# Kernel optimization log

Hardware: AMD Instinct MI355X
Metric: run time of the kernel (lower is better)

Reference implementation:

```python
import jax, jax.numpy as jnp
import numpy as np

B, T, C = 128, 64, 66
S, L, W = 512, 2, 32  # state_size, num_layers, window_size


def _gru_cell(x, h, Wih, Whh, bih, bhh):
    # PyTorch GRU cell. x:[B,in], h:[B,S]; gate order r,z,n.
    gi = x @ Wih.T + bih  # [B,3S]
    gh = h @ Whh.T + bhh
    ir, iz, inn = jnp.split(gi, 3, axis=-1)
    hr, hz, hn = jnp.split(gh, 3, axis=-1)
    r = jax.nn.sigmoid(ir + hr)
    z = jax.nn.sigmoid(iz + hz)
    n = jnp.tanh(inn + r * hn)
    return (1.0 - z) * n + z * h


def setup_inputs() -> dict:
    key = jax.random.key(0)
    ks = jax.random.split(key, 14)
    sc = 0.02
    inp = {
        'x': jax.random.normal(ks[0], (B, T, C), dtype=jnp.float32),
        'Wih0': jax.random.normal(ks[1], (3 * S, C), dtype=jnp.float32) * sc,
        'Whh0': jax.random.normal(ks[2], (3 * S, S), dtype=jnp.float32) * sc,
        'bih0': jax.random.normal(ks[3], (3 * S,), dtype=jnp.float32) * sc,
        'bhh0': jax.random.normal(ks[4], (3 * S,), dtype=jnp.float32) * sc,
        'Wih1': jax.random.normal(ks[5], (3 * S, S), dtype=jnp.float32) * sc,
        'Whh1': jax.random.normal(ks[6], (3 * S, S), dtype=jnp.float32) * sc,
        'bih1': jax.random.normal(ks[7], (3 * S,), dtype=jnp.float32) * sc,
        'bhh1': jax.random.normal(ks[8], (3 * S,), dtype=jnp.float32) * sc,
        'Wt': jax.random.normal(ks[9], (1, W), dtype=jnp.float32) * sc,   # temporal_fc_last: Linear(W,1)
        'bt': jnp.zeros((1,), dtype=jnp.float32),
        'Ws': jax.random.normal(ks[10], (C, S), dtype=jnp.float32) * sc,  # spatial_fc: Linear(S,C)
        'bs': jnp.zeros((C,), dtype=jnp.float32),
    }
    return inp


def reference(x, Wih0, Whh0, bih0, bhh0, Wih1, Whh1, bih1, bhh1, Wt, bt, Ws, bs):
    Bx, Tx, Cx = x.shape
    h0 = jnp.zeros((Bx, S), dtype=x.dtype)
    h1 = jnp.zeros((Bx, S), dtype=x.dtype)

    def stack_step(h0, h1, xt):
        h0 = _gru_cell(xt, h0, Wih0, Whh0, bih0, bhh0)
        h1 = _gru_cell(h0, h1, Wih1, Whh1, bih1, bhh1)
        return h0, h1

    # ---- encoder over x[:, :-1, :] ----
    def enc_step(carry, xt):
        h0, h1 = stack_step(carry[0], carry[1], xt)
        return (h0, h1), h1

    (h0, h1), enc_out = jax.lax.scan(enc_step, (h0, h1), x[:, :-1, :].transpose(1, 0, 2))
    # enc_out: [T-1, B, S]; sliding window of the last W encoder outputs: [B, W, S]
    window = enc_out[-W:].transpose(1, 0, 2)

    def dec_step(carry, _):
        h0, h1, win, dinp = carry  # dinp: [B, C]
        h0, h1 = stack_step(h0, h1, dinp)
        win = jnp.concatenate([win[:, 1:, :], h1[:, None, :]], axis=1)  # slide window
        # temporal_fc_last over time axis (after b n d -> b d n): [B, S]
        temp = jnp.einsum('bws,w->bs', win, Wt[0]) + bt[0]
        out = temp @ Ws.T + bs  # spatial_fc: [B, C]
        new_frame = out + dinp  # recursive residual
        return (h0, h1, win, new_frame), new_frame

    init = (h0, h1, window, x[:, -1, :])
    _, frames = jax.lax.scan(dec_step, init, None, length=Tx)  # [T, B, C]
    return frames.transpose(1, 0, 2)  # [B, T, C]
```

## Files before the change

kernel.cpp:

```cpp
#include <hip/hip_runtime.h>
#include <stdint.h>

typedef unsigned short u16;
typedef uint32_t u32;
typedef __attribute__((ext_vector_type(8))) short short8;
typedef __attribute__((ext_vector_type(4))) float floatx4;

constexpr int BB = 128;
constexpr int TT = 64;
constexpr int CC = 66;
constexpr int CPAD = 96;
constexpr int SS = 512;
constexpr int NGATE = 1536;
constexpr int NGRP = 8;
constexpr int GBLK = 16;
constexpr int GS = 16 * SS;
constexpr int NEG = -1000000;

__device__ __forceinline__ u16 f2bf(float f) {
    u32 u = __float_as_uint(f);
    u32 r = (u + 0x7fffu + ((u >> 16) & 1u)) >> 16;
    return (u16)r;
}
__device__ __forceinline__ float bf2f(u16 h) {
    return __uint_as_float(((u32)h) << 16);
}
__device__ __forceinline__ float sigm(float x) { return 1.f / (1.f + __expf(-x)); }
__device__ __forceinline__ float tanh_f(float x) { return 1.f - 2.f / (1.f + __expf(2.f * x)); }

__device__ __forceinline__ void store_u16_cc(u16* p, u16 v) {
    asm volatile("global_store_short %0, %1, off sc0 sc1"
                 :: "v"(p), "v"((u32)v) : "memory");
}
__device__ __forceinline__ void load_issue_cc(const u16* p, short8& d) {
    asm volatile("global_load_dwordx4 %0, %1, off sc0 sc1"
                 : "=v"(d) : "v"(p));
}
__device__ __forceinline__ void vm_drain() {
    asm volatile("s_waitcnt vmcnt(0)" ::: "memory");
}

__global__ void prep1_kernel(const float* __restrict__ x,
                             const float* __restrict__ Wih0,
                             const float* __restrict__ Whh0,
                             const float* __restrict__ Wih1,
                             const float* __restrict__ Whh1,
                             const float* __restrict__ Ws,
                             u16* __restrict__ xbf, u16* __restrict__ wi0,
                             u16* __restrict__ wh0, u16* __restrict__ wi1,
                             u16* __restrict__ wh1, u16* __restrict__ wsb)
{
    const int N_xbf = BB * TT * CPAD;
    const int N_wi0 = NGATE * CPAD;
    const int N_whh = NGATE * SS;
    const int N_wsb = 80 * SS;
    const long total = (long)N_xbf + N_wi0 + 3L * N_whh + N_wsb;
    for (long i = (long)blockIdx.x * blockDim.x + threadIdx.x; i < total;
         i += (long)gridDim.x * blockDim.x) {
        long idx = i;
        if (idx < N_xbf) {
            int c = idx % CPAD; int bt = idx / CPAD;
            float v = (c < CC) ? x[(long)bt * CC + c] : 0.f;
            xbf[idx] = f2bf(v); continue;
        }
        idx -= N_xbf;
        if (idx < N_wi0) {
            int c = idx % CPAD; int n = idx / CPAD;
            float v = (c < CC) ? Wih0[(long)n * CC + c] : 0.f;
            wi0[idx] = f2bf(v); continue;
        }
        idx -= N_wi0;
        if (idx < N_whh) { wh0[idx] = f2bf(Whh0[idx]); continue; }
        idx -= N_whh;
        if (idx < N_whh) { wi1[idx] = f2bf(Wih1[idx]); continue; }
        idx -= N_whh;
        if (idx < N_whh) { wh1[idx] = f2bf(Whh1[idx]); continue; }
        idx -= N_whh;
        {
            int s = idx % SS; int c = idx / SS;
            wsb[idx] = (c < CC) ? f2bf(Ws[(long)c * SS + s]) : (u16)0;
        }
    }
}

__global__ void prep2_kernel(const float* __restrict__ x,
                             const float* __restrict__ Wih0,
                             const float* __restrict__ Ws,
                             const float* __restrict__ bs,
                             u16* __restrict__ Mbf, float* __restrict__ c0vec,
                             float* __restrict__ gi0i)
{
    const long NM = (long)NGATE * SS;
    const long NC = NGATE;
    const long NG = (long)BB * NGATE;
    const long total = NM + NC + NG;
    for (long i = (long)blockIdx.x * blockDim.x + threadIdx.x; i < total;
         i += (long)gridDim.x * blockDim.x) {
        long idx = i;
        if (idx < NM) {
            int s = idx % SS; int g = idx / SS;
            float acc = 0.f;
            for (int c = 0; c < CC; ++c)
                acc += Wih0[(long)g * CC + c] * Ws[(long)c * SS + s];
            Mbf[idx] = f2bf(acc); continue;
        }
        idx -= NM;
        if (idx < NC) {
            int g = idx;
            float acc = 0.f;
            for (int c = 0; c < CC; ++c) acc += Wih0[(long)g * CC + c] * bs[c];
            c0vec[g] = acc; continue;
        }
        idx -= NC;
        {
            int g = idx % NGATE; int b = idx / NGATE;
            float acc = 0.f;
            const float* xl = x + ((long)b * TT + (TT - 1)) * CC;
            for (int c = 0; c < CC; ++c) acc += xl[c] * Wih0[(long)g * CC + c];
            gi0i[idx] = acc;
        }
    }
}

__device__ __forceinline__ void wait2(const int* __restrict__ f0, int t0,
                                      const int* __restrict__ f1, int t1) {
    const int lane = threadIdx.x & 63;
    const int* p = (lane < 32) ? (f0 + lane) : (f1 + (lane - 32));
    const int tgt = (lane < 32) ? t0 : t1;
    for (;;) {
        int v = __hip_atomic_load(p, __ATOMIC_RELAXED, __HIP_MEMORY_SCOPE_AGENT);
        if (__all(v >= tgt)) break;
        __builtin_amdgcn_s_sleep(1);
    }
    asm volatile("" ::: "memory");
}

__device__ __forceinline__ void set_flag(int* f, int v) {
    if ((threadIdx.x & 63) == 0)
        __hip_atomic_store(f, v, __ATOMIC_RELAXED, __HIP_MEMORY_SCOPE_AGENT);
}

__device__ __forceinline__ void load_afrags(const u16* __restrict__ st,
                                            int l15, int quad, short8* a) {
#pragma unroll
    for (int kc = 0; kc < 16; ++kc)
        load_issue_cc(st + (long)l15 * SS + kc * 32 + quad * 8, a[kc]);
}

#define MFMA_BF16(a, wp, acc) \
    acc = __builtin_amdgcn_mfma_f32_16x16x32_bf16(a, *(const short8*)(wp), acc, 0, 0, 0)

__device__ __forceinline__ void mm3_reg(const short8* a,
                                        const u16* __restrict__ w0,
                                        const u16* __restrict__ w1,
                                        const u16* __restrict__ w2,
                                        floatx4& A0, floatx4& A1, floatx4& A2) {
#pragma unroll
    for (int kc = 0; kc < 16; ++kc) {
        const int k = kc << 5;
        MFMA_BF16(a[kc], w0 + k, A0);
        MFMA_BF16(a[kc], w1 + k, A1);
        MFMA_BF16(a[kc], w2 + k, A2);
    }
}

template <int K>
__device__ __forceinline__ void mm3_g(const u16* __restrict__ aP,
                                      const u16* __restrict__ w0,
                                      const u16* __restrict__ w1,
                                      const u16* __restrict__ w2,
                                      floatx4& A0, floatx4& A1, floatx4& A2) {
#pragma unroll
    for (int k = 0; k < K; k += 32) {
        short8 a = *(const short8*)(aP + k);
        MFMA_BF16(a, w0 + k, A0);
        MFMA_BF16(a, w1 + k, A1);
        MFMA_BF16(a, w2 + k, A2);
    }
}

__global__ __launch_bounds__(256, 1) void persist_kernel(
    const u16* __restrict__ xbf,
    const u16* __restrict__ wi0, const u16* __restrict__ wh0,
    const u16* __restrict__ wi1, const u16* __restrict__ wh1,
    const u16* __restrict__ Mbf,
    const float* __restrict__ bih0, const float* __restrict__ bhh0,
    const float* __restrict__ bih1, const float* __restrict__ bhh1,
    const float* __restrict__ c0vec, const float* __restrict__ gi0i,
    const float* __restrict__ Wt, const float* __restrict__ bt,
    u16* __restrict__ h0buf,
    u16* __restrict__ h1buf,
    u16* __restrict__ tstage,
    u16* __restrict__ temps,
    int* __restrict__ gflags)
{
    const int tid = threadIdx.x;
    const int wave = tid >> 6, lane = tid & 63;
    const int l15 = lane & 15, quad = lane >> 4;
    const int grp = blockIdx.x >> 4, rank = blockIdx.x & 15;
    const int b0g = grp * 16;
    const int wsub = wave & 1;
    const int sg = rank * 32 + wsub * 16 + l15;
    const bool l0w = wave < 2;

    u16* const h0g = h0buf + (long)grp * 4 * GS;
    u16* const h1g = h1buf + (long)grp * 2 * GS;
    u16* const tsg = tstage + (long)grp * 2 * GS;
    int* const f0 = gflags + grp * 64;
    int* const f1 = f0 + 32;
    const int myflag = rank * 2 + wsub;

    float bir, biz, bin, bhn;
    float c0r = 0.f, c0z = 0.f, c0n = 0.f;
    float hf[4] = {0.f, 0.f, 0.f, 0.f};
    float gi[12];
    float wt[32]; float btv = 0.f;
    u32 wreg[4][16];
#pragma unroll
    for (int r = 0; r < 4; ++r)
#pragma unroll
        for (int i = 0; i < 16; ++i) wreg[r][i] = 0u;

    if (l0w) {
        bir = bih0[sg] + bhh0[sg];
        biz = bih0[512 + sg] + bhh0[512 + sg];
        bin = bih0[1024 + sg];
        bhn = bhh0[1024 + sg];
        c0r = c0vec[sg]; c0z = c0vec[512 + sg]; c0n = c0vec[1024 + sg];
#pragma unroll
        for (int g3 = 0; g3 < 3; ++g3)
#pragma unroll
            for (int r = 0; r < 4; ++r)
                gi[g3 * 4 + r] =
                    gi0i[(long)(b0g + quad * 4 + r) * NGATE + g3 * 512 + sg];
    } else {
        bir = bih1[sg] + bhh1[sg];
        biz = bih1[512 + sg] + bhh1[512 + sg];
        bin = bih1[1024 + sg];
        bhn = bhh1[1024 + sg];
#pragma unroll
        for (int j = 0; j < 32; ++j) wt[j] = Wt[j];
        btv = bt[0];
    }

    const u16 *wiR, *wiZ, *wiN, *whR, *whZ, *whN, *mR, *mZ, *mN;
    if (l0w) {
        wiR = wi0 + (long)sg * CPAD + quad * 8;
        wiZ = wi0 + (long)(512 + sg) * CPAD + quad * 8;
        wiN = wi0 + (long)(1024 + sg) * CPAD + quad * 8;
        whR = wh0 + (long)sg * SS + quad * 8;
        whZ = wh0 + (long)(512 + sg) * SS + quad * 8;
        whN = wh0 + (long)(1024 + sg) * SS + quad * 8;
        mR = Mbf + (long)sg * SS + quad * 8;
        mZ = Mbf + (long)(512 + sg) * SS + quad * 8;
        mN = Mbf + (long)(1024 + sg) * SS + quad * 8;
    } else {
        wiR = wi1 + (long)sg * SS + quad * 8;
        wiZ = wi1 + (long)(512 + sg) * SS + quad * 8;
        wiN = wi1 + (long)(1024 + sg) * SS + quad * 8;
        whR = wh1 + (long)sg * SS + quad * 8;
        whZ = wh1 + (long)(512 + sg) * SS + quad * 8;
        whN = wh1 + (long)(1024 + sg) * SS + quad * 8;
        mR = mZ = mN = nullptr;
    }

    short8 fa[16], fb[16];

    if (l0w) {
        for (int t = 0; t < 63; ++t) {
            wait2(f0, t, f1, t - 3);
            load_afrags(h0g + (long)(t & 3) * GS, l15, quad, fa);
            floatx4 aR = {0,0,0,0}, aZ = aR, aNI = aR, aNH = aR;
            const u16* aP = xbf + ((long)(b0g + l15) * TT + t) * CPAD + quad * 8;
            mm3_g<CPAD>(aP, wiR, wiZ, wiN, aR, aZ, aNI);
            vm_drain();
            mm3_reg(fa, whR, whZ, whN, aR, aZ, aNH);
            u16* dst = h0g + (long)((t + 1) & 3) * GS;
#pragma unroll
            for (int r = 0; r < 4; ++r) {
                float rr = sigm(aR[r] + bir);
                float zz = sigm(aZ[r] + biz);
                float nn = tanh_f(aNI[r] + bin + rr * (aNH[r] + bhn));
                float hv = (1.f - zz) * nn + zz * hf[r];
                hf[r] = hv;
                store_u16_cc(dst + (long)(quad * 4 + r) * SS + sg, f2bf(hv));
            }
            vm_drain();
            set_flag(f0 + myflag, t + 1);
        }
        for (int d = 0; d < 64; ++d) {
            const int t = 63 + d;
            wait2(f0, t, f1, (d > 0) ? t : 60);
            if (d > 0) {
                load_afrags(tsg + (long)((d - 1) & 1) * GS, l15, quad, fb);
            }
            load_afrags(h0g + (long)(t & 3) * GS, l15, quad, fa);
            vm_drain();
            if (d > 0) {
                floatx4 tR = {0,0,0,0}, tZ = tR, tN = tR;
                mm3_reg(fb, mR, mZ, mN, tR, tZ, tN);
#pragma unroll
                for (int r = 0; r < 4; ++r) {
                    gi[r] += tR[r] + c0r;
                    gi[4 + r] += tZ[r] + c0z;
                    gi[8 + r] += tN[r] + c0n;
                }
            }
            floatx4 hR = {0,0,0,0}, hZ = hR, hN4 = hR;
            mm3_reg(fa, whR, whZ, whN, hR, hZ, hN4);
            u16* dst = h0g + (long)((t + 1) & 3) * GS;
#pragma unroll
            for (int r = 0; r < 4; ++r) {
                float rr = sigm(gi[r] + hR[r] + bir);
                float zz = sigm(gi[4 + r] + hZ[r] + biz);
                float nn = tanh_f(gi[8 + r] + bin + rr * (hN4[r] + bhn));
                float hv = (1.f - zz) * nn + zz * hf[r];
                hf[r] = hv;
                store_u16_cc(dst + (long)(quad * 4 + r) * SS + sg, f2bf(hv));
            }
            vm_drain();
            set_flag(f0 + myflag, t + 1);
        }
    } else {
        for (int u = 0; u < 63; ++u) {
            wait2(f0, u + 1, f1, u);
            load_afrags(h0g + (long)((u + 1) & 3) * GS, l15, quad, fa);
            load_afrags(h1g + (long)(u & 1) * GS, l15, quad, fb);
            vm_drain();
            floatx4 aR = {0,0,0,0}, aZ = aR, aNI = aR, aNH = aR;
            mm3_reg(fa, wiR, wiZ, wiN, aR, aZ, aNI);
            mm3_reg(fb, whR, whZ, whN, aR, aZ, aNH);
            u16* dst = h1g + (long)((u + 1) & 1) * GS;
#pragma unroll
            for (int r = 0; r < 4; ++r) {
                float rr = sigm(aR[r] + bir);
                float zz = sigm(aZ[r] + biz);
                float nn = tanh_f(aNI[r] + bin + rr * (aNH[r] + bhn));
                float hv = (1.f - zz) * nn + zz * hf[r];
                hf[r] = hv;
                u16 hb = f2bf(hv);
                store_u16_cc(dst + (long)(quad * 4 + r) * SS + sg, hb);
#pragma unroll
                for (int i = 0; i < 15; ++i)
                    wreg[r][i] = (wreg[r][i] >> 16) | (wreg[r][i + 1] << 16);
                wreg[r][15] = (wreg[r][15] >> 16) | ((u32)hb << 16);
            }
            vm_drain();
            set_flag(f1 + myflag, u + 1);
        }
        for (int d = 0; d < 64; ++d) {
            const int u = 63 + d;
            wait2(f0, u + 1, f1, u);
            load_afrags(h0g + (long)((u + 1) & 3) * GS, l15, quad, fa);
            load_afrags(h1g + (long)(u & 1) * GS, l15, quad, fb);
            vm_drain();
            floatx4 aR = {0,0,0,0}, aZ = aR, aNI = aR, aNH = aR;
            mm3_reg(fa, wiR, wiZ, wiN, aR, aZ, aNI);
            mm3_reg(fb, whR, whZ, whN, aR, aZ, aNH);
            u16* dst = h1g + (long)((u + 1) & 1) * GS;
            u16* tdst = tsg + (long)(d & 1) * GS;
            u16* tOut = temps + (long)d * (BB * SS);
#pragma unroll
            for (int r = 0; r < 4; ++r) {
                float rr = sigm(aR[r] + bir);
                float zz = sigm(aZ[r] + biz);
                float nn = tanh_f(aNI[r] + bin + rr * (aNH[r] + bhn));
                float hv = (1.f - zz) * nn + zz * hf[r];
                hf[r] = hv;
                u16 hb = f2bf(hv);
                store_u16_cc(dst + (long)(quad * 4 + r) * SS + sg, hb);
#pragma unroll
                for (int i = 0; i < 15; ++i)
                    wreg[r][i] = (wreg[r][i] >> 16) | (wreg[r][i + 1] << 16);
                wreg[r][15] = (wreg[r][15] >> 16) | ((u32)hb << 16);
                float tacc = btv;
#pragma unroll
                for (int i = 0; i < 16; ++i) {
                    u32 wv = wreg[r][i];
                    tacc += __uint_as_float(wv << 16) * wt[2 * i];
                    tacc += __uint_as_float(wv & 0xffff0000u) * wt[2 * i + 1];
                }
                u16 tb = f2bf(tacc);
                store_u16_cc(tdst + (long)(quad * 4 + r) * SS + sg, tb);
                tOut[(long)(b0g + quad * 4 + r) * SS + sg] = tb;
            }
            vm_drain();
            set_flag(f1 + myflag, u + 1);
        }
    }
}

__global__ __launch_bounds__(256) void frames_kernel(
    const u16* __restrict__ temps, const float* __restrict__ x,
    const u16* __restrict__ wsb, const float* __restrict__ bs,
    float* __restrict__ outp)
{
    const int b = blockIdx.x, tid = threadIdx.x;
    const int wave = tid >> 6, lane = tid & 63;
    const int l15 = lane & 15, quad = lane >> 4;
    __shared__ float P[64][81];

    const int e0 = wave * 16;
    floatx4 acc[5];
#pragma unroll
    for (int ct = 0; ct < 5; ++ct) acc[ct] = (floatx4){0.f, 0.f, 0.f, 0.f};
    const u16* aBase =
        temps + (long)(e0 + l15) * (BB * SS) + (long)b * SS + quad * 8;
#pragma unroll
    for (int kc = 0; kc < 16; ++kc) {
        short8 a = *(const short8*)(aBase + kc * 32);
#pragma unroll
        for (int ct = 0; ct < 5; ++ct) {
            const u16* wp = wsb + (long)(ct * 16 + l15) * SS + quad * 8 + kc * 32;
            MFMA_BF16(a, wp, acc[ct]);
        }
    }
#pragma unroll
    for (int ct = 0; ct < 5; ++ct)
#pragma unroll
        for (int r = 0; r < 4; ++r)
            P[e0 + quad * 4 + r][ct * 16 + l15] = acc[ct][r];
    __syncthreads();

    const int c = tid;
    if (c < CC) {
        float cum = x[((long)b * TT + (TT - 1)) * CC + c];
        const float bsv = bs[c];
        for (int e = 0; e < TT; ++e) {
            cum += P[e][c] + bsv;
            outp[(long)b * TT * CC + (long)e * CC + c] = cum;
        }
    }
}

extern "C" void kernel_launch(void* const* d_in, const int* in_sizes, int n_in,
                              void* d_out, int out_size, void* d_ws, size_t ws_size,
                              hipStream_t stream)
{
    const float* x    = (const float*)d_in[0];
    const float* Wih0 = (const float*)d_in[1];
    const float* Whh0 = (const float*)d_in[2];
    const float* bih0 = (const float*)d_in[3];
    const float* bhh0 = (const float*)d_in[4];
    const float* Wih1 = (const float*)d_in[5];
    const float* Whh1 = (const float*)d_in[6];
    const float* bih1 = (const float*)d_in[7];
    const float* bhh1 = (const float*)d_in[8];
    const float* Wt   = (const float*)d_in[9];
    const float* bt   = (const float*)d_in[10];
    const float* Ws   = (const float*)d_in[11];
    const float* bs   = (const float*)d_in[12];
    float* outp = (float*)d_out;

    char* p = (char*)d_ws;
    auto alloc = [&](size_t bytes) -> char* {
        char* r = p; p += (bytes + 255) & ~(size_t)255; return r;
    };
    u16* h0buf = (u16*)alloc((size_t)NGRP * 4 * GS * 2);
    u16* h1buf = (u16*)alloc((size_t)NGRP * 2 * GS * 2);
    u16* tstage = (u16*)alloc((size_t)NGRP * 2 * GS * 2);
    u16* xbf = (u16*)alloc((size_t)BB * TT * CPAD * 2);
    u16* wi0 = (u16*)alloc((size_t)NGATE * CPAD * 2);
    u16* wh0 = (u16*)alloc((size_t)NGATE * SS * 2);
    u16* wi1 = (u16*)alloc((size_t)NGATE * SS * 2);
    u16* wh1 = (u16*)alloc((size_t)NGATE * SS * 2);
    u16* Mbf = (u16*)alloc((size_t)NGATE * SS * 2);
    u16* wsb = (u16*)alloc((size_t)80 * SS * 2);
    float* c0vec = (float*)alloc((size_t)NGATE * 4);
    float* gi0i  = (float*)alloc((size_t)BB * NGATE * 4);
    u16* temps = (u16*)alloc((size_t)TT * BB * SS * 2);
    int* gflags = (int*)alloc((size_t)NGRP * 64 * 4);

    hipMemsetAsync(h0buf, 0, (size_t)NGRP * 4 * GS * 2, stream);
    hipMemsetAsync(h1buf, 0, (size_t)NGRP * 2 * GS * 2, stream);
    hipMemsetAsync(gflags, 0, (size_t)NGRP * 64 * 4, stream);

    prep1_kernel<<<1024, 256, 0, stream>>>(x, Wih0, Whh0, Wih1, Whh1, Ws,
                                           xbf, wi0, wh0, wi1, wh1, wsb);
    prep2_kernel<<<1024, 256, 0, stream>>>(x, Wih0, Ws, bs, Mbf, c0vec, gi0i);

    persist_kernel<<<NGRP * GBLK, 256, 0, stream>>>(
        xbf, wi0, wh0, wi1, wh1, Mbf, bih0, bhh0, bih1, bhh1,
        c0vec, gi0i, Wt, bt, h0buf, h1buf, tstage, temps, gflags);

    frames_kernel<<<BB, 256, 0, stream>>>(temps, x, wsb, bs, outp);
}
```

Before: 2.705 ms.

## Co-locate GRU groups per XCD, coalesce state stores via LDS, pad flags

Remaps blocks so each 16-block group lands on one XCD (blockIdx & 7), then detects at runtime whether all blocks of a group share an XCD and, if so, uses sc0-only (no system-coherent sc1) loads and stores for the exchanged hidden state. Hidden and temporal outputs are staged through LDS so each wave writes 128-bit stores instead of scattered 16-bit stores. Flags are padded to separate cache lines, and the layer-0 input projection is issued before the flag wait to overlap it with synchronisation. This adds a startup handshake and duplicates the loop body for both coherence modes, and relies on the hardware XCD placement assumption for correctness of the fast path.

After: 4.083 ms. 51.0% more time.

```diff
diff --git a/kernel.cpp b/kernel.cpp
--- a/kernel.cpp
+++ b/kernel.cpp
@@ -15,7 +15,8 @@
 constexpr int NGRP = 8;
 constexpr int GBLK = 16;
 constexpr int GS = 16 * SS;
-constexpr int NEG = -1000000;
+
+template <bool B> struct BoolC { static constexpr bool value = B; };
 
 __device__ __forceinline__ u16 f2bf(float f) {
     u32 u = __float_as_uint(f);
@@ -28,16 +29,40 @@
 __device__ __forceinline__ float sigm(float x) { return 1.f / (1.f + __expf(-x)); }
 __device__ __forceinline__ float tanh_f(float x) { return 1.f - 2.f / (1.f + __expf(2.f * x)); }
 
-__device__ __forceinline__ void store_u16_cc(u16* p, u16 v) {
-    asm volatile("global_store_short %0, %1, off sc0 sc1"
-                 :: "v"(p), "v"((u32)v) : "memory");
-}
-__device__ __forceinline__ void load_issue_cc(const u16* p, short8& d) {
-    asm volatile("global_load_dwordx4 %0, %1, off sc0 sc1"
-                 : "=v"(d) : "v"(p));
+template <bool F> __device__ __forceinline__ void st128(u16* p, short8 v) {
+    if (F) asm volatile("global_store_dwordx4 %0, %1, off sc0"
+                        :: "v"(p), "v"(v) : "memory");
+    else   asm volatile("global_store_dwordx4 %0, %1, off sc0 sc1"
+                        :: "v"(p), "v"(v) : "memory");
+}
+template <bool F> __device__ __forceinline__ void ld128(const u16* p, short8& d) {
+    if (F) asm volatile("global_load_dwordx4 %0, %1, off sc0"
+                        : "=v"(d) : "v"(p));
+    else   asm volatile("global_load_dwordx4 %0, %1, off sc0 sc1"
+                        : "=v"(d) : "v"(p));
 }
 __device__ __forceinline__ void vm_drain() {
     asm volatile("s_waitcnt vmcnt(0)" ::: "memory");
+}
+__device__ __forceinline__ void lds_drain() {
+    asm volatile("s_waitcnt lgkmcnt(0)" ::: "memory");
+}
+
+__device__ __forceinline__ void set_flag(int* f, int v) {
+    if ((threadIdx.x & 63) == 0)
+        __hip_atomic_store(f, v, __ATOMIC_RELAXED, __HIP_MEMORY_SCOPE_AGENT);
+}
+__device__ __forceinline__ void wait2(const int* __restrict__ f0, int t0,
+                                      const int* __restrict__ f1, int t1) {
+    const int lane = threadIdx.x & 63;
+    const int* p = (lane < 32) ? (f0 + lane * 16) : (f1 + (lane - 32) * 16);
+    const int tgt = (lane < 32) ? t0 : t1;
+    for (;;) {
+        int v = __hip_atomic_load(p, __ATOMIC_RELAXED, __HIP_MEMORY_SCOPE_AGENT);
+        if (__all(v >= tgt)) break;
+        __builtin_amdgcn_s_sleep(1);
+    }
+    asm volatile("" ::: "memory");
 }
 
 __global__ void prep1_kernel(const float* __restrict__ x,
@@ -122,29 +147,12 @@
     }
 }
 
-__device__ __forceinline__ void wait2(const int* __restrict__ f0, int t0,
-                                      const int* __restrict__ f1, int t1) {
-    const int lane = threadIdx.x & 63;
-    const int* p = (lane < 32) ? (f0 + lane) : (f1 + (lane - 32));
-    const int tgt = (lane < 32) ? t0 : t1;
-    for (;;) {
-        int v = __hip_atomic_load(p, __ATOMIC_RELAXED, __HIP_MEMORY_SCOPE_AGENT);
-        if (__all(v >= tgt)) break;
-        __builtin_amdgcn_s_sleep(1);
-    }
-    asm volatile("" ::: "memory");
-}
-
-__device__ __forceinline__ void set_flag(int* f, int v) {
-    if ((threadIdx.x & 63) == 0)
-        __hip_atomic_store(f, v, __ATOMIC_RELAXED, __HIP_MEMORY_SCOPE_AGENT);
-}
-
+template <bool F>
 __device__ __forceinline__ void load_afrags(const u16* __restrict__ st,
                                             int l15, int quad, short8* a) {
 #pragma unroll
     for (int kc = 0; kc < 16; ++kc)
-        load_issue_cc(st + (long)l15 * SS + kc * 32 + quad * 8, a[kc]);
+        ld128<F>(st + (long)l15 * SS + kc * 32 + quad * 8, a[kc]);
 }
 
 #define MFMA_BF16(a, wp, acc) \
@@ -192,23 +200,46 @@
     u16* __restrict__ h1buf,
     u16* __restrict__ tstage,
     u16* __restrict__ temps,
-    int* __restrict__ gflags)
+    int* __restrict__ gflags,
+    int* __restrict__ initfl)
 {
+    __shared__ __align__(16) u16 tile[4][2][256];
+
     const int tid = threadIdx.x;
     const int wave = tid >> 6, lane = tid & 63;
     const int l15 = lane & 15, quad = lane >> 4;
-    const int grp = blockIdx.x >> 4, rank = blockIdx.x & 15;
+    const int grp = blockIdx.x & 7, rank = blockIdx.x >> 3;
     const int b0g = grp * 16;
     const int wsub = wave & 1;
-    const int sg = rank * 32 + wsub * 16 + l15;
+    const int sg0 = rank * 32 + wsub * 16;
+    const int sg = sg0 + l15;
     const bool l0w = wave < 2;
 
     u16* const h0g = h0buf + (long)grp * 4 * GS;
     u16* const h1g = h1buf + (long)grp * 2 * GS;
     u16* const tsg = tstage + (long)grp * 2 * GS;
-    int* const f0 = gflags + grp * 64;
-    int* const f1 = f0 + 32;
+    int* const f0 = gflags + grp * 1024;
+    int* const f1 = f0 + 512;
     const int myflag = rank * 2 + wsub;
+
+    int xcd = __builtin_amdgcn_s_getreg((31 << 11) | 20) & 0xff;
+    if (tid == 0)
+        __hip_atomic_store(initfl + (grp * 16 + rank) * 16, xcd + 1,
+                           __ATOMIC_RELAXED, __HIP_MEMORY_SCOPE_AGENT);
+    __syncthreads();
+    bool fast;
+    {
+        const int* p = initfl + (grp * 16 + (lane & 15)) * 16;
+        int v;
+        for (;;) {
+            v = __hip_atomic_load(p, __ATOMIC_RELAXED,
+                                  __HIP_MEMORY_SCOPE_AGENT);
+            if (__all(v != 0)) break;
+            __builtin_amdgcn_s_sleep(8);
+        }
+        int first = __shfl(v, 0);
+        fast = __all(v == first);
+    }
 
     float bir, biz, bin, bhn;
     float c0r = 0.f, c0z = 0.f, c0n = 0.f;
@@ -264,130 +295,136 @@
         mR = mZ = mN = nullptr;
     }
 
-    short8 fa[16], fb[16];
-
-    if (l0w) {
-        for (int t = 0; t < 63; ++t) {
-            wait2(f0, t, f1, t - 3);
-            load_afrags(h0g + (long)(t & 3) * GS, l15, quad, fa);
-            floatx4 aR = {0,0,0,0}, aZ = aR, aNI = aR, aNH = aR;
-            const u16* aP = xbf + ((long)(b0g + l15) * TT + t) * CPAD + quad * 8;
-            mm3_g<CPAD>(aP, wiR, wiZ, wiN, aR, aZ, aNI);
-            vm_drain();
-            mm3_reg(fa, whR, whZ, whN, aR, aZ, aNH);
-            u16* dst = h0g + (long)((t + 1) & 3) * GS;
-#pragma unroll
-            for (int r = 0; r < 4; ++r) {
-                float rr = sigm(aR[r] + bir);
-                float zz = sigm(aZ[r] + biz);
-                float nn = tanh_f(aNI[r] + bin + rr * (aNH[r] + bhn));
-                float hv = (1.f - zz) * nn + zz * hf[r];
-                hf[r] = hv;
-                store_u16_cc(dst + (long)(quad * 4 + r) * SS + sg, f2bf(hv));
+    const int srow = lane >> 1, shalf = lane & 1;
+    u16* const myTileH = &tile[wave][0][0];
+    u16* const myTileT = &tile[wave][1][0];
+
+    auto run = [&](auto fc) {
+        constexpr bool F = decltype(fc)::value;
+        short8 fa[16], fb[16];
+        if (l0w) {
+#pragma clang loop unroll(disable)
+            for (int t = 0; t < 63; ++t) {
+                floatx4 aR = {0,0,0,0}, aZ = aR, aNI = aR, aNH = aR;
+                const u16* aP =
+                    xbf + ((long)(b0g + l15) * TT + t) * CPAD + quad * 8;
+                mm3_g<CPAD>(aP, wiR, wiZ, wiN, aR, aZ, aNI);
+                wait2(f0, t, f1, t - 3);
+                load_afrags<F>(h0g + (long)(t & 3) * GS, l15, quad, fa);
+                vm_drain();
+                mm3_reg(fa, whR, whZ, whN, aR, aZ, aNH);
+#pragma unroll
+                for (int r = 0; r < 4; ++r) {
+                    float rr = sigm(aR[r] + bir);
+                    float zz = sigm(aZ[r] + biz);
+                    float nn = tanh_f(aNI[r] + bin + rr * (aNH[r] + bhn));
+                    float hv = (1.f - zz) * nn + zz * hf[r];
+                    hf[r] = hv;
+                    myTileH[(quad * 4 + r) * 16 + l15] = f2bf(hv);
+                }
+                lds_drain();
+                if (lane < 32) {
+                    short8 v = *(const short8*)(myTileH + srow * 16 + shalf * 8);
+                    st128<F>(h0g + (long)((t + 1) & 3) * GS +
+                             (long)srow * SS + sg0 + shalf * 8, v);
+                }
+                vm_drain();
+                set_flag(f0 + myflag * 16, t + 1);
             }
-            vm_drain();
-            set_flag(f0 + myflag, t + 1);
-        }
-        for (int d = 0; d < 64; ++d) {
-            const int t = 63 + d;
-            wait2(f0, t, f1, (d > 0) ? t : 60);
-            if (d > 0) {
-                load_afrags(tsg + (long)((d - 1) & 1) * GS, l15, quad, fb);
+#pragma clang loop unroll(disable)
+            for (int d = 0; d < 64; ++d) {
+                const int t = 63 + d;
+                wait2(f0, t, f1, (d > 0) ? t : 60);
+                load_afrags<F>(h0g + (long)(t & 3) * GS, l15, quad, fa);
+                if (d > 0)
+                    load_afrags<F>(tsg + (long)((d - 1) & 1) * GS, l15, quad, fb);
+                vm_drain();
+                if (d > 0) {
+                    floatx4 tR = {0,0,0,0}, tZ = tR, tN = tR;
+                    mm3_reg(fb, mR, mZ, mN, tR, tZ, tN);
+#pragma unroll
+                    for (int r = 0; r < 4; ++r) {
+                        gi[r] += tR[r] + c0r;
+                        gi[4 + r] += tZ[r] + c0z;
+                        gi[8 + r] += tN[r] + c0n;
+                    }
+                }
+                floatx4 hR = {0,0,0,0}, hZ = hR, hN4 = hR;
+                mm3_reg(fa, whR, whZ, whN, hR, hZ, hN4);
+#pragma unroll
+                for (int r = 0; r < 4; ++r) {
+                    float rr = sigm(gi[r] + hR[r] + bir);
+                    float zz = sigm(gi[4 + r] + hZ[r] + biz);
+                    float nn = tanh_f(gi[8 + r] + bin + rr * (hN4[r] + bhn));
+                    float hv = (1.f - zz) * nn + zz * hf[r];
+                    hf[r] = hv;
+                    myTileH[(quad * 4 + r) * 16 + l15] = f2bf(hv);
+                }
+                lds_drain();
+                if (lane < 32) {
+                    short8 v = *(const short8*)(myTileH + srow * 16 + shalf * 8);
+                    st128<F>(h0g + (long)((t + 1) & 3) * GS +
+                             (long)srow * SS + sg0 + shalf * 8, v);
+                }
+                vm_drain();
+                set_flag(f0 + myflag * 16, t + 1);
             }
-            load_afrags(h0g + (long)(t & 3) * GS, l15, quad, fa);
-            vm_drain();
-            if (d > 0) {
-                floatx4 tR = {0,0,0,0}, tZ = tR, tN = tR;
-                mm3_reg(fb, mR, mZ, mN, tR, tZ, tN);
+        } else {
+#pragma clang loop unroll(disable)
+            for (int u = 0; u < 127; ++u) {
+                const bool dec = (u >= 63);
+                const int d = u - 63;
+                wait2(f0, u + 1, f1, u);
+                load_afrags<F>(h0g + (long)((u + 1) & 3) * GS, l15, quad, fa);
+                load_afrags<F>(h1g + (long)(u & 1) * GS, l15, quad, fb);
+                vm_drain();
+                floatx4 aR = {0,0,0,0}, aZ = aR, aNI = aR, aNH = aR;
+                mm3_reg(fa, wiR, wiZ, wiN, aR, aZ, aNI);
+                mm3_reg(fb, whR, whZ, whN, aR, aZ, aNH);
 #pragma unroll
                 for (int r = 0; r < 4; ++r) {
-                    gi[r] += tR[r] + c0r;
-                    gi[4 + r] += tZ[r] + c0z;
-                    gi[8 + r] += tN[r] + c0n;
-                }
+                    float rr = sigm(aR[r] + bir);
+                    float zz = sigm(aZ[r] + biz);
+                    float nn = tanh_f(aNI[r] + bin + rr * (aNH[r] + bhn));
+                    float hv = (1.f - zz) * nn + zz * hf[r];
+                    hf[r] = hv;
+                    u16 hb = f2bf(hv);
+                    myTileH[(quad * 4 + r) * 16 + l15] = hb;
+#pragma unroll
+                    for (int i = 0; i < 15; ++i)
+                        wreg[r][i] = (wreg[r][i] >> 16) | (wreg[r][i + 1] << 16);
+                    wreg[r][15] = (wreg[r][15] >> 16) | ((u32)hb << 16);
+                    if (dec) {
+                        float tacc = btv;
+#pragma unroll
+                        for (int i = 0; i < 16; ++i) {
+                            u32 wv = wreg[r][i];
+                            tacc += __uint_as_float(wv << 16) * wt[2 * i];
+                            tacc += __uint_as_float(wv & 0xffff0000u) * wt[2 * i + 1];
+                        }
+                        myTileT[(quad * 4 + r) * 16 + l15] = f2bf(tacc);
+                    }
+                }
+                lds_drain();
+                if (lane < 32) {
+                    short8 v = *(const short8*)(myTileH + srow * 16 + shalf * 8);
+                    st128<F>(h1g + (long)((u + 1) & 1) * GS +
+                             (long)srow * SS + sg0 + shalf * 8, v);
+                    if (dec) {
+                        short8 w = *(const short8*)(myTileT + srow * 16 + shalf * 8);
+                        st128<F>(tsg + (long)(d & 1) * GS +
+                                 (long)srow * SS + sg0 + shalf * 8, w);
+                        *(short8*)(temps + (long)d * (BB * SS) +
+                                   (long)(b0g + srow) * SS + sg0 + shalf * 8) = w;
+                    }
+                }
+                vm_drain();
+                set_flag(f1 + myflag * 16, u + 1);
             }
-            floatx4 hR = {0,0,0,0}, hZ = hR, hN4 = hR;
-            mm3_reg(fa, whR, whZ, whN, hR, hZ, hN4);
-            u16* dst = h0g + (long)((t + 1) & 3) * GS;
-#pragma unroll
-            for (int r = 0; r < 4; ++r) {
-                float rr = sigm(gi[r] + hR[r] + bir);
-                float zz = sigm(gi[4 + r] + hZ[r] + biz);
-                float nn = tanh_f(gi[8 + r] + bin + rr * (hN4[r] + bhn));
-                float hv = (1.f - zz) * nn + zz * hf[r];
-                hf[r] = hv;
-                store_u16_cc(dst + (long)(quad * 4 + r) * SS + sg, f2bf(hv));
-            }
-            vm_drain();
-            set_flag(f0 + myflag, t + 1);
-        }
-    } else {
-        for (int u = 0; u < 63; ++u) {
-            wait2(f0, u + 1, f1, u);
-            load_afrags(h0g + (long)((u + 1) & 3) * GS, l15, quad, fa);
-            load_afrags(h1g + (long)(u & 1) * GS, l15, quad, fb);
-            vm_drain();
-            floatx4 aR = {0,0,0,0}, aZ = aR, aNI = aR, aNH = aR;
-            mm3_reg(fa, wiR, wiZ, wiN, aR, aZ, aNI);
-            mm3_reg(fb, whR, whZ, whN, aR, aZ, aNH);
-            u16* dst = h1g + (long)((u + 1) & 1) * GS;
-#pragma unroll
-            for (int r = 0; r < 4; ++r) {
-                float rr = sigm(aR[r] + bir);
-                float zz = sigm(aZ[r] + biz);
-                float nn = tanh_f(aNI[r] + bin + rr * (aNH[r] + bhn));
-                float hv = (1.f - zz) * nn + zz * hf[r];
-                hf[r] = hv;
-                u16 hb = f2bf(hv);
-                store_u16_cc(dst + (long)(quad * 4 + r) * SS + sg, hb);
-#pragma unroll
-                for (int i = 0; i < 15; ++i)
-                    wreg[r][i] = (wreg[r][i] >> 16) | (wreg[r][i + 1] << 16);
-                wreg[r][15] = (wreg[r][15] >> 16) | ((u32)hb << 16);
-            }
-            vm_drain();
-            set_flag(f1 + myflag, u + 1);
-        }
-        for (int d = 0; d < 64; ++d) {
-            const int u = 63 + d;
-            wait2(f0, u + 1, f1, u);
-            load_afrags(h0g + (long)((u + 1) & 3) * GS, l15, quad, fa);
-            load_afrags(h1g + (long)(u & 1) * GS, l15, quad, fb);
-            vm_drain();
-            floatx4 aR = {0,0,0,0}, aZ = aR, aNI = aR, aNH = aR;
-            mm3_reg(fa, wiR, wiZ, wiN, aR, aZ, aNI);
-            mm3_reg(fb, whR, whZ, whN, aR, aZ, aNH);
-            u16* dst = h1g + (long)((u + 1) & 1) * GS;
-            u16* tdst = tsg + (long)(d & 1) * GS;
-            u16* tOut = temps + (long)d * (BB * SS);
-#pragma unroll
-            for (int r = 0; r < 4; ++r) {
-                float rr = sigm(aR[r] + bir);
-                float zz = sigm(aZ[r] + biz);
-                float nn = tanh_f(aNI[r] + bin + rr * (aNH[r] + bhn));
-                float hv = (1.f - zz) * nn + zz * hf[r];
-                hf[r] = hv;
-                u16 hb = f2bf(hv);
-                store_u16_cc(dst + (long)(quad * 4 + r) * SS + sg, hb);
-#pragma unroll
-                for (int i = 0; i < 15; ++i)
-                    wreg[r][i] = (wreg[r][i] >> 16) | (wreg[r][i + 1] << 16);
-                wreg[r][15] = (wreg[r][15] >> 16) | ((u32)hb << 16);
-                float tacc = btv;
-#pragma unroll
-                for (int i = 0; i < 16; ++i) {
-                    u32 wv = wreg[r][i];
-                    tacc += __uint_as_float(wv << 16) * wt[2 * i];
-                    tacc += __uint_as_float(wv & 0xffff0000u) * wt[2 * i + 1];
-                }
-                u16 tb = f2bf(tacc);
-                store_u16_cc(tdst + (long)(quad * 4 + r) * SS + sg, tb);
-                tOut[(long)(b0g + quad * 4 + r) * SS + sg] = tb;
-            }
-            vm_drain();
-            set_flag(f1 + myflag, u + 1);
-        }
-    }
+        }
+    };
+    if (fast) run(BoolC<true>{});
+    else      run(BoolC<false>{});
 }
 
 __global__ __launch_bounds__(256) void frames_kernel(
@@ -469,11 +506,13 @@
     float* c0vec = (float*)alloc((size_t)NGATE * 4);
     float* gi0i  = (float*)alloc((size_t)BB * NGATE * 4);
     u16* temps = (u16*)alloc((size_t)TT * BB * SS * 2);
-    int* gflags = (int*)alloc((size_t)NGRP * 64 * 4);
+    int* gflags = (int*)alloc((size_t)NGRP * 1024 * 4);
+    int* initfl = (int*)alloc((size_t)NGRP * 16 * 16 * 4);
 
     hipMemsetAsync(h0buf, 0, (size_t)NGRP * 4 * GS * 2, stream);
     hipMemsetAsync(h1buf, 0, (size_t)NGRP * 2 * GS * 2, stream);
-    hipMemsetAsync(gflags, 0, (size_t)NGRP * 64 * 4, stream);
+    hipMemsetAsync(gflags, 0, (size_t)NGRP * 1024 * 4, stream);
+    hipMemsetAsync(initfl, 0, (size_t)NGRP * 16 * 16 * 4, stream);
 
     prep1_kernel<<<1024, 256, 0, stream>>>(x, Wih0, Whh0, Wih1, Whh1, Ws,
                                            xbf, wi0, wh0, wi1, wh1, wsb);
@@ -481,7 +520,7 @@
 
     persist_kernel<<<NGRP * GBLK, 256, 0, stream>>>(
         xbf, wi0, wh0, wi1, wh1, Mbf, bih0, bhh0, bih1, bhh1,
-        c0vec, gi0i, Wt, bt, h0buf, h1buf, tstage, temps, gflags);
+        c0vec, gi0i, Wt, bt, h0buf, h1buf, tstage, temps, gflags, initfl);
 
     frames_kernel<<<BB, 256, 0, stream>>>(temps, x, wsb, bs, outp);
 }
```
